# Performance work log

Hardware: AMD Instinct MI355X
Metric: run time of the kernel (lower is better)

Reference implementation:

```python
import jax, jax.numpy as jnp
import numpy as np

N = 50000      # nodes
E = 800000     # edges (before self loops)
IN = 32        # in_channels
HID = 32       # hidden_channels per head
HEADS = 4
OUT = 8        # out_channels (classes)
HD = HID * HEADS  # 128
NEG_SLOPE = 0.2
LN_EPS = 1e-5


def setup_inputs() -> dict:
    key = jax.random.key(0)
    ks = jax.random.split(key, 20)
    g = lambda k, shape, s=0.05: (jax.random.normal(k, shape, jnp.float32) * s)
    return {
        "x": jax.random.normal(ks[0], (N, IN), jnp.float32),
        "edge_index": jax.random.randint(ks[1], (2, E), 0, N, dtype=jnp.int32),
        # layer 0 GATConv (IN -> HID per head, HEADS heads, concat)
        "W0": g(ks[2], (IN, HD)),
        "a_src0": g(ks[3], (HEADS, HID)),
        "a_dst0": g(ks[4], (HEADS, HID)),
        "b0": jnp.zeros((HD,), jnp.float32),
        # skip projection for layer 0 (IN != HD)
        "skipW0": g(ks[5], (IN, HD)),
        "skipb0": jnp.zeros((HD,), jnp.float32),
        # LayerNorm 0
        "g0": jnp.ones((HD,), jnp.float32),
        "be0": jnp.zeros((HD,), jnp.float32),
        # layer 1 GATConv (HD -> HID per head, HEADS heads, concat)
        "W1": g(ks[6], (HD, HD)),
        "a_src1": g(ks[7], (HEADS, HID)),
        "a_dst1": g(ks[8], (HEADS, HID)),
        "b1": jnp.zeros((HD,), jnp.float32),
        # LayerNorm 1
        "g1": jnp.ones((HD,), jnp.float32),
        "be1": jnp.zeros((HD,), jnp.float32),
        # final GATConv (HD -> OUT, 1 head, no concat)
        "W2": g(ks[9], (HD, OUT)),
        "a_src2": g(ks[10], (1, OUT)),
        "a_dst2": g(ks[11], (1, OUT)),
        "b2": jnp.zeros((OUT,), jnp.float32),
    }


def _gat_conv(h_in, W, a_src, a_dst, b, src, dst, heads, C, concat):
    """PyG-style GATConv (eval mode, self-loops already in src/dst)."""
    n = h_in.shape[0]
    h = (h_in @ W).reshape(n, heads, C)                 # [N, H, C]
    s = jnp.sum(h * a_src[None], axis=-1)               # [N, H]
    d = jnp.sum(h * a_dst[None], axis=-1)               # [N, H]
    e = jax.nn.leaky_relu(s[src] + d[dst], NEG_SLOPE)   # [E, H]
    # segment softmax over incoming edges of each destination node
    m = jax.ops.segment_max(e, dst, num_segments=n)
    m = jnp.where(jnp.isfinite(m), m, 0.0)
    ex = jnp.exp(e - m[dst])
    den = jax.ops.segment_sum(ex, dst, num_segments=n)
    alpha = ex / (den[dst] + 1e-16)                     # [E, H]
    msg = h[src] * alpha[:, :, None]                    # [E, H, C]
    out = jax.ops.segment_sum(msg, dst, num_segments=n) # [N, H, C]
    out = out.reshape(n, heads * C) if concat else out.mean(axis=1)
    return out + b


def _layer_norm(x, g, b):
    mu = x.mean(axis=-1, keepdims=True)
    var = jnp.mean(jnp.square(x - mu), axis=-1, keepdims=True)
    return (x - mu) * jax.lax.rsqrt(var + LN_EPS) * g + b


def reference(x, edge_index, W0, a_src0, a_dst0, b0, skipW0, skipb0, g0, be0,
              W1, a_src1, a_dst1, b1, g1, be1, W2, a_src2, a_dst2, b2):
    n = x.shape[0]
    loop = jnp.arange(n, dtype=edge_index.dtype)
    src = jnp.concatenate([edge_index[0], loop])
    dst = jnp.concatenate([edge_index[1], loop])

    # layer 0: GATConv + projected residual + LN + ELU (dropout = identity, eval)
    h = _gat_conv(x, W0, a_src0, a_dst0, b0, src, dst, HEADS, HID, True)
    h = h + (x @ skipW0 + skipb0)
    h = jax.nn.elu(_layer_norm(h, g0, be0))

    # layer 1: GATConv + identity residual (dims match) + LN + ELU
    h1 = _gat_conv(h, W1, a_src1, a_dst1, b1, src, dst, HEADS, HID, True)
    h1 = h1 + h
    h1 = jax.nn.elu(_layer_norm(h1, g1, be1))

    # final layer: 1 head, mean (concat=False)
    return _gat_conv(h1, W2, a_src2, a_dst2, b2, src, dst, 1, OUT, False)
```

## Files before the change

### kernel.cpp

```cpp
#include <hip/hip_runtime.h>
#include <hip/hip_fp16.h>
#include <math.h>

#define N_NODES 50000
#define N_EDGES 800000
#define E2 (N_EDGES + N_NODES)
#define HD 128
#define OUT_C 8
#define NEG_SLOPE 0.2f
#define LN_EPS 1e-5f
#define NB_SCAN ((N_NODES + 255) / 256)

__device__ __forceinline__ float lrelu(float x) { return x > 0.f ? x : NEG_SLOPE * x; }
__device__ __forceinline__ void fma4(float4& a, float s, const float4& w) {
  a.x += s * w.x; a.y += s * w.y; a.z += s * w.z; a.w += s * w.w;
}
__device__ __forceinline__ float dot4(const float4& a, const float4& b) {
  return a.x * b.x + a.y * b.y + a.z * b.z + a.w * b.w;
}

__global__ void hist_k(const int* __restrict__ ei, int* __restrict__ counts) {
  int e = blockIdx.x * 256 + threadIdx.x;
  if (e >= E2) return;
  int d = (e < N_EDGES) ? ei[N_EDGES + e] : (e - N_EDGES);
  atomicAdd(&counts[d], 1);
}

__global__ void scan1_k(const int* __restrict__ counts, int* __restrict__ incl,
                        int* __restrict__ bsum, int n) {
  int tid = threadIdx.x; int gid = blockIdx.x * 256 + tid;
  int v = (gid < n) ? counts[gid] : 0;
  int lane = tid & 63, wv = tid >> 6;
  int x = v;
  #pragma unroll
  for (int off = 1; off < 64; off <<= 1) { int t = __shfl_up(x, off); if (lane >= off) x += t; }
  __shared__ int ws[4];
  if (lane == 63) ws[wv] = x;
  __syncthreads();
  for (int w = 0; w < wv; ++w) x += ws[w];
  incl[gid] = x;
  if (tid == 255) bsum[blockIdx.x] = x;
}

__global__ void scan2_k(const int* __restrict__ bsum, int* __restrict__ boffs, int nb) {
  int tid = threadIdx.x;
  int v = (tid < nb) ? bsum[tid] : 0;
  int lane = tid & 63, wv = tid >> 6;
  int x = v;
  #pragma unroll
  for (int off = 1; off < 64; off <<= 1) { int t = __shfl_up(x, off); if (lane >= off) x += t; }
  __shared__ int ws[4];
  if (lane == 63) ws[wv] = x;
  __syncthreads();
  for (int w = 0; w < wv; ++w) x += ws[w];
  if (tid < nb) boffs[tid] = x - v;
}

__global__ void scan3_k(const int* __restrict__ counts, const int* __restrict__ incl,
                        const int* __restrict__ boffs, int* __restrict__ row_start,
                        int* __restrict__ cursor, int n) {
  int gid = blockIdx.x * 256 + threadIdx.x;
  if (gid < n) {
    int r = incl[gid] - counts[gid] + boffs[blockIdx.x];
    row_start[gid] = r; cursor[gid] = r;
  }
  if (gid == 0) row_start[n] = E2;
}

__global__ void scatter_k(const int* __restrict__ ei, int* __restrict__ cursor,
                          int* __restrict__ csr_src) {
  int e = blockIdx.x * 256 + threadIdx.x;
  if (e >= E2) return;
  int s, d;
  if (e < N_EDGES) { s = ei[e]; d = ei[N_EDGES + e]; } else { s = e - N_EDGES; d = s; }
  int pos = atomicAdd(&cursor[d], 1);
  csr_src[pos] = s;
}

#define NPB0 16
__global__ __launch_bounds__(256) void gemm0_k(
    const float* __restrict__ x, const float* __restrict__ W0,
    const float* __restrict__ skipW, const float* __restrict__ skipb,
    const float* __restrict__ asrc, const float* __restrict__ adst,
    __half* __restrict__ h0, float* __restrict__ skip,
    float* __restrict__ s0, float* __restrict__ d0) {
  __shared__ float Ws[32 * 128];
  __shared__ float Ss[32 * 128];
  __shared__ float xs[NPB0][32];
  int tid = threadIdx.x;
  for (int i = tid; i < 32 * 128 / 4; i += 256) {
    ((float4*)Ws)[i] = ((const float4*)W0)[i];
    ((float4*)Ss)[i] = ((const float4*)skipW)[i];
  }
  int nb = blockIdx.x * NPB0;
  for (int i = tid; i < NPB0 * 32 / 4; i += 256) {
    int node = nb + (i >> 3);
    ((float4*)xs)[i] = (node < N_NODES) ? ((const float4*)x)[node * 8 + (i & 7)]
                                        : make_float4(0, 0, 0, 0);
  }
  __syncthreads();
  int j = tid >> 5;
  int cg = tid & 31;
  float4 aH[2] = {{0,0,0,0},{0,0,0,0}};
  float4 aS[2] = {{0,0,0,0},{0,0,0,0}};
  #pragma unroll 4
  for (int k = 0; k < 32; ++k) {
    float4 w  = ((const float4*)Ws)[k * 32 + cg];
    float4 wk = ((const float4*)Ss)[k * 32 + cg];
    float x0 = xs[j][k], x1 = xs[j + 8][k];
    fma4(aH[0], x0, w);  fma4(aH[1], x1, w);
    fma4(aS[0], x0, wk); fma4(aS[1], x1, wk);
  }
  float4 as4 = ((const float4*)asrc)[cg];
  float4 ad4 = ((const float4*)adst)[cg];
  float4 sb4 = ((const float4*)skipb)[cg];
  #pragma unroll
  for (int t = 0; t < 2; ++t) {
    int n = nb + j + t * 8;
    if (n < N_NODES) {
      float4 h = aH[t];
      union { __half2 h2[2]; uint2 u; } pk;
      pk.h2[0] = __floats2half2_rn(h.x, h.y);
      pk.h2[1] = __floats2half2_rn(h.z, h.w);
      ((uint2*)h0)[(size_t)n * 32 + cg] = pk.u;
      float4 sk = aS[t];
      sk.x += sb4.x; sk.y += sb4.y; sk.z += sb4.z; sk.w += sb4.w;
      ((float4*)skip)[n * 32 + cg] = sk;
      float sv = h.x * as4.x + h.y * as4.y + h.z * as4.z + h.w * as4.w;
      float dv = h.x * ad4.x + h.y * ad4.y + h.z * ad4.z + h.w * ad4.w;
      #pragma unroll
      for (int off = 1; off < 8; off <<= 1) { sv += __shfl_xor(sv, off); dv += __shfl_xor(dv, off); }
      if ((cg & 7) == 0) { s0[n * 4 + (cg >> 3)] = sv; d0[n * 4 + (cg >> 3)] = dv; }
    }
  }
}

#define G1N 64
__global__ __launch_bounds__(256) void gemm1_k(
    const float* __restrict__ hin, const float* __restrict__ W1,
    const float* __restrict__ asrc, const float* __restrict__ adst,
    __half* __restrict__ hpre, float* __restrict__ s1, float* __restrict__ d1) {
  __shared__ float xs[G1N][132];
  __shared__ float Ws[64][128];
  int tid = threadIdx.x;
  int nb = blockIdx.x * G1N;
  for (int i = tid; i < G1N * 32; i += 256) {
    int ln = i >> 5, k4 = i & 31;
    int node = nb + ln;
    float4 v = (node < N_NODES) ? ((const float4*)hin)[(size_t)node * 32 + k4]
                                : make_float4(0, 0, 0, 0);
    *(float4*)&xs[ln][k4 * 4] = v;
  }
  int cg = tid & 15, jn = tid >> 4;
  int c0 = cg * 8, n0 = jn * 4;
  float4 acc[4][2] = {};
  for (int ph = 0; ph < 2; ++ph) {
    __syncthreads();
    for (int i = tid; i < 64 * 32; i += 256)
      ((float4*)Ws)[i] = ((const float4*)W1)[ph * 2048 + i];
    __syncthreads();
    #pragma unroll 4
    for (int k = 0; k < 64; ++k) {
      float4 w0 = *(const float4*)&Ws[k][c0];
      float4 w1 = *(const float4*)&Ws[k][c0 + 4];
      int kk = ph * 64 + k;
      #pragma unroll
      for (int i = 0; i < 4; ++i) {
        float xv = xs[n0 + i][kk];
        fma4(acc[i][0], xv, w0);
        fma4(acc[i][1], xv, w1);
      }
    }
  }
  float4 a0 = *(const float4*)&asrc[c0], a1 = *(const float4*)&asrc[c0 + 4];
  float4 d0_ = *(const float4*)&adst[c0], d1_ = *(const float4*)&adst[c0 + 4];
  int head = cg >> 2;
  #pragma unroll
  for (int i = 0; i < 4; ++i) {
    int n = nb + n0 + i;
    if (n < N_NODES) {
      union { __half2 h2[4]; uint4 u; } pk;
      pk.h2[0] = __floats2half2_rn(acc[i][0].x, acc[i][0].y);
      pk.h2[1] = __floats2half2_rn(acc[i][0].z, acc[i][0].w);
      pk.h2[2] = __floats2half2_rn(acc[i][1].x, acc[i][1].y);
      pk.h2[3] = __floats2half2_rn(acc[i][1].z, acc[i][1].w);
      ((uint4*)hpre)[(size_t)n * 16 + cg] = pk.u;
      float sv = dot4(acc[i][0], a0) + dot4(acc[i][1], a1);
      float dv = dot4(acc[i][0], d0_) + dot4(acc[i][1], d1_);
      sv += __shfl_xor(sv, 1); sv += __shfl_xor(sv, 2);
      dv += __shfl_xor(dv, 1); dv += __shfl_xor(dv, 2);
      if ((cg & 3) == 0) { s1[n * 4 + head] = sv; d1[n * 4 + head] = dv; }
    }
  }
}

__global__ __launch_bounds__(256) void gemm2_k(
    const float* __restrict__ hin, const float* __restrict__ W2,
    const float* __restrict__ asrc, const float* __restrict__ adst,
    float* __restrict__ h2, float* __restrict__ s2, float* __restrict__ d2) {
  __shared__ float Ws[128 * 8];
  __shared__ float as[8], ad[8];
  int tid = threadIdx.x;
  for (int i = tid; i < 128 * 8 / 4; i += 256) ((float4*)Ws)[i] = ((const float4*)W2)[i];
  if (tid < 8) { as[tid] = asrc[tid]; ad[tid] = adst[tid]; }
  __syncthreads();
  int node = blockIdx.x * 256 + tid;
  if (node >= N_NODES) return;
  const float4* row = (const float4*)(hin + (size_t)node * 128);
  float acc[8] = {0, 0, 0, 0, 0, 0, 0, 0};
  #pragma unroll 4
  for (int k4 = 0; k4 < 32; ++k4) {
    float4 xv = row[k4];
    const float* wb = &Ws[k4 * 32];
    #pragma unroll
    for (int c = 0; c < 8; ++c)
      acc[c] += xv.x * wb[c] + xv.y * wb[8 + c] + xv.z * wb[16 + c] + xv.w * wb[24 + c];
  }
  float sv = 0.f, dv = 0.f;
  #pragma unroll
  for (int c = 0; c < 8; ++c) {
    h2[(size_t)node * 8 + c] = acc[c];
    sv += acc[c] * as[c]; dv += acc[c] * ad[c];
  }
  s2[node] = sv; d2[node] = dv;
}

__global__ __launch_bounds__(256) void agg_k(
    const int* __restrict__ row_start, const int* __restrict__ csr_src,
    const __half* __restrict__ hfeat, const float* __restrict__ sarr,
    const float* __restrict__ darr, const float* __restrict__ bias,
    const float* __restrict__ resid, const float* __restrict__ gamma,
    const float* __restrict__ beta, float* __restrict__ outf) {
  int lane = threadIdx.x & 63;
  int n = blockIdx.x * 4 + (threadIdx.x >> 6);
  if (n >= N_NODES) return;
  int rs = row_start[n], re = row_start[n + 1];
  float4 dn4 = ((const float4*)darr)[n];
  float m0 = -INFINITY, m1 = -INFINITY, m2 = -INFINITY, m3 = -INFINITY;
  for (int p = rs + lane; p < re; p += 64) {
    int src = csr_src[p];
    float4 sv = ((const float4*)sarr)[src];
    m0 = fmaxf(m0, lrelu(sv.x + dn4.x)); m1 = fmaxf(m1, lrelu(sv.y + dn4.y));
    m2 = fmaxf(m2, lrelu(sv.z + dn4.z)); m3 = fmaxf(m3, lrelu(sv.w + dn4.w));
  }
  #pragma unroll
  for (int off = 32; off; off >>= 1) {
    m0 = fmaxf(m0, __shfl_xor(m0, off)); m1 = fmaxf(m1, __shfl_xor(m1, off));
    m2 = fmaxf(m2, __shfl_xor(m2, off)); m3 = fmaxf(m3, __shfl_xor(m3, off));
  }
  int head = lane >> 4;
  float mh = head == 0 ? m0 : head == 1 ? m1 : head == 2 ? m2 : m3;
  float dh = head == 0 ? dn4.x : head == 1 ? dn4.y : head == 2 ? dn4.z : dn4.w;
  const __half2* hf2 = (const __half2*)hfeat;
  float den = 0.f, acc0 = 0.f, acc1 = 0.f;
  int p = rs;
  for (; p + 1 < re; p += 2) {
    int sA = csr_src[p], sB = csr_src[p + 1];
    float shA = sarr[sA * 4 + head], shB = sarr[sB * 4 + head];
    __half2 hA = hf2[(size_t)sA * 64 + lane];
    __half2 hB = hf2[(size_t)sB * 64 + lane];
    float exA = __expf(lrelu(shA + dh) - mh);
    float exB = __expf(lrelu(shB + dh) - mh);
    den += exA + exB;
    float2 a = __half22float2(hA), b = __half22float2(hB);
    acc0 += exA * a.x + exB * b.x;
    acc1 += exA * a.y + exB * b.y;
  }
  if (p < re) {
    int sA = csr_src[p];
    float shA = sarr[sA * 4 + head];
    __half2 hA = hf2[(size_t)sA * 64 + lane];
    float exA = __expf(lrelu(shA + dh) - mh);
    den += exA;
    float2 a = __half22float2(hA);
    acc0 += exA * a.x; acc1 += exA * a.y;
  }
  float rden = 1.f / (den + 1e-16f);
  int c0 = lane * 2;
  float o0 = acc0 * rden + bias[c0]     + resid[(size_t)n * 128 + c0];
  float o1 = acc1 * rden + bias[c0 + 1] + resid[(size_t)n * 128 + c0 + 1];
  float s = o0 + o1;
  #pragma unroll
  for (int off = 32; off; off >>= 1) s += __shfl_xor(s, off);
  float mu = s * (1.f / 128.f);
  float v0 = o0 - mu, v1 = o1 - mu;
  float vv = v0 * v0 + v1 * v1;
  #pragma unroll
  for (int off = 32; off; off >>= 1) vv += __shfl_xor(vv, off);
  float rstd = rsqrtf(vv * (1.f / 128.f) + LN_EPS);
  float y0 = v0 * rstd * gamma[c0]     + beta[c0];
  float y1 = v1 * rstd * gamma[c0 + 1] + beta[c0 + 1];
  y0 = y0 > 0.f ? y0 : expm1f(y0);
  y1 = y1 > 0.f ? y1 : expm1f(y1);
  ((float2*)outf)[(size_t)n * 64 + lane] = make_float2(y0, y1);
}

__global__ __launch_bounds__(256) void agg2_k(
    const int* __restrict__ row_start, const int* __restrict__ csr_src,
    const float* __restrict__ h2, const float* __restrict__ s2,
    const float* __restrict__ d2, const float* __restrict__ b2,
    float* __restrict__ outf) {
  int lane = threadIdx.x & 63;
  int n = blockIdx.x * 4 + (threadIdx.x >> 6);
  if (n >= N_NODES) return;
  int rs = row_start[n], re = row_start[n + 1];
  float dn = d2[n];
  float mx = -INFINITY;
  for (int p = rs + lane; p < re; p += 64)
    mx = fmaxf(mx, lrelu(s2[csr_src[p]] + dn));
  #pragma unroll
  for (int off = 32; off; off >>= 1) mx = fmaxf(mx, __shfl_xor(mx, off));
  float den = 0.f;
  float acc[8] = {0, 0, 0, 0, 0, 0, 0, 0};
  for (int p = rs + lane; p < re; p += 64) {
    int src = csr_src[p];
    float e = lrelu(s2[src] + dn);
    float ex = __expf(e - mx);
    den += ex;
    float4 hA = ((const float4*)h2)[src * 2];
    float4 hB = ((const float4*)h2)[src * 2 + 1];
    acc[0] += ex * hA.x; acc[1] += ex * hA.y; acc[2] += ex * hA.z; acc[3] += ex * hA.w;
    acc[4] += ex * hB.x; acc[5] += ex * hB.y; acc[6] += ex * hB.z; acc[7] += ex * hB.w;
  }
  #pragma unroll
  for (int off = 32; off; off >>= 1) {
    den += __shfl_xor(den, off);
    #pragma unroll
    for (int i = 0; i < 8; ++i) acc[i] += __shfl_xor(acc[i], off);
  }
  if (lane == 0) {
    float r = 1.f / (den + 1e-16f);
    #pragma unroll
    for (int i = 0; i < 8; ++i) outf[(size_t)n * 8 + i] = acc[i] * r + b2[i];
  }
}

extern "C" void kernel_launch(void* const* d_in, const int* in_sizes, int n_in,
                              void* d_out, int out_size, void* d_ws, size_t ws_size,
                              hipStream_t stream) {
  const float* x      = (const float*)d_in[0];
  const int*   ei     = (const int*)d_in[1];
  const float* W0     = (const float*)d_in[2];
  const float* a_src0 = (const float*)d_in[3];
  const float* a_dst0 = (const float*)d_in[4];
  const float* b0     = (const float*)d_in[5];
  const float* skipW0 = (const float*)d_in[6];
  const float* skipb0 = (const float*)d_in[7];
  const float* g0     = (const float*)d_in[8];
  const float* be0    = (const float*)d_in[9];
  const float* W1     = (const float*)d_in[10];
  const float* a_src1 = (const float*)d_in[11];
  const float* a_dst1 = (const float*)d_in[12];
  const float* b1     = (const float*)d_in[13];
  const float* g1     = (const float*)d_in[14];
  const float* be1    = (const float*)d_in[15];
  const float* W2     = (const float*)d_in[16];
  const float* a_src2 = (const float*)d_in[17];
  const float* a_dst2 = (const float*)d_in[18];
  const float* b2     = (const float*)d_in[19];
  float* out = (float*)d_out;

  char* w = (char*)d_ws;
  auto alloc = [&](size_t bytes) -> char* {
    char* p = w; w += (bytes + 255) & ~(size_t)255; return p;
  };
  int* counts    = (int*)alloc((size_t)N_NODES * 4);
  int* row_start = (int*)alloc((size_t)(N_NODES + 1) * 4);
  int* cursor    = (int*)alloc((size_t)N_NODES * 4);
  int* incl      = (int*)alloc((size_t)NB_SCAN * 256 * 4);
  int* bsum      = (int*)alloc((size_t)NB_SCAN * 4);
  int* boffs     = (int*)alloc((size_t)NB_SCAN * 4);
  int* csr_src   = (int*)alloc((size_t)E2 * 4);
  float* A       = (float*)alloc((size_t)N_NODES * 128 * 4);
  float* B       = (float*)alloc((size_t)N_NODES * 128 * 4);
  float* C       = (float*)alloc((size_t)N_NODES * 128 * 4);
  float* s0v = (float*)alloc((size_t)N_NODES * 4 * 4);
  float* d0v = (float*)alloc((size_t)N_NODES * 4 * 4);
  float* s1v = (float*)alloc((size_t)N_NODES * 4 * 4);
  float* d1v = (float*)alloc((size_t)N_NODES * 4 * 4);
  float* s2v = (float*)alloc((size_t)N_NODES * 4);
  float* d2v = (float*)alloc((size_t)N_NODES * 4);

  hipMemsetAsync(counts, 0, (size_t)N_NODES * 4, stream);
  int egrid = (E2 + 255) / 256;
  hist_k<<<egrid, 256, 0, stream>>>(ei, counts);
  scan1_k<<<NB_SCAN, 256, 0, stream>>>(counts, incl, bsum, N_NODES);
  scan2_k<<<1, 256, 0, stream>>>(bsum, boffs, NB_SCAN);
  scan3_k<<<NB_SCAN, 256, 0, stream>>>(counts, incl, boffs, row_start, cursor, N_NODES);
  scatter_k<<<egrid, 256, 0, stream>>>(ei, cursor, csr_src);

  int ngrid4 = (N_NODES + 3) / 4;
  gemm0_k<<<(N_NODES + NPB0 - 1) / NPB0, 256, 0, stream>>>(
      x, W0, skipW0, skipb0, a_src0, a_dst0, (__half*)A, B, s0v, d0v);
  agg_k<<<ngrid4, 256, 0, stream>>>(row_start, csr_src, (const __half*)A, s0v, d0v, b0, B, g0, be0, C);
  gemm1_k<<<(N_NODES + G1N - 1) / G1N, 256, 0, stream>>>(C, W1, a_src1, a_dst1, (__half*)B, s1v, d1v);
  agg_k<<<ngrid4, 256, 0, stream>>>(row_start, csr_src, (const __half*)B, s1v, d1v, b1, C, g1, be1, A);
  gemm2_k<<<(N_NODES + 255) / 256, 256, 0, stream>>>(A, W2, a_src2, a_dst2, B, s2v, d2v);
  agg2_k<<<ngrid4, 256, 0, stream>>>(row_start, csr_src, B, s2v, d2v, b2, out);
}
```

Baseline: 422.6 us.

## Drop softmax max pass and share per-edge exp weights via LDS

Removes the segment-max pass in both aggregation kernels and computes exp of the leaky-relu logits without max subtraction. In the 128-wide aggregation, each wave computes the per-edge exps for all four heads once per 64-edge chunk and stages them and the source indices in LDS, instead of every lane re-gathering scores. This removes one full edge pass and redundant gathers. It risks overflow if logits become large, because the max shift that kept exp bounded is gone.

```diff
diff --git a/kernel.cpp b/kernel.cpp
--- a/kernel.cpp
+++ b/kernel.cpp
@@ -225,58 +225,65 @@
   s2[node] = sv; d2[node] = dv;
 }
 
+template<int LAYER>
 __global__ __launch_bounds__(256) void agg_k(
     const int* __restrict__ row_start, const int* __restrict__ csr_src,
     const __half* __restrict__ hfeat, const float* __restrict__ sarr,
     const float* __restrict__ darr, const float* __restrict__ bias,
     const float* __restrict__ resid, const float* __restrict__ gamma,
     const float* __restrict__ beta, float* __restrict__ outf) {
+  __shared__ float exs[4][64 * 4];
+  __shared__ int   srs[4][64];
   int lane = threadIdx.x & 63;
-  int n = blockIdx.x * 4 + (threadIdx.x >> 6);
+  int wv = threadIdx.x >> 6;
+  int n = blockIdx.x * 4 + wv;
   if (n >= N_NODES) return;
   int rs = row_start[n], re = row_start[n + 1];
   float4 dn4 = ((const float4*)darr)[n];
-  float m0 = -INFINITY, m1 = -INFINITY, m2 = -INFINITY, m3 = -INFINITY;
-  for (int p = rs + lane; p < re; p += 64) {
-    int src = csr_src[p];
-    float4 sv = ((const float4*)sarr)[src];
-    m0 = fmaxf(m0, lrelu(sv.x + dn4.x)); m1 = fmaxf(m1, lrelu(sv.y + dn4.y));
-    m2 = fmaxf(m2, lrelu(sv.z + dn4.z)); m3 = fmaxf(m3, lrelu(sv.w + dn4.w));
+  int head = lane >> 4;
+  int c0 = lane * 2;
+  const __half2* hf2 = (const __half2*)hfeat;
+  float4 denv = {0.f, 0.f, 0.f, 0.f};
+  float acc0 = 0.f, acc1 = 0.f;
+  for (int base = rs; base < re; base += 64) {
+    int cnt = re - base; if (cnt > 64) cnt = 64;
+    if (lane < cnt) {
+      int src = csr_src[base + lane];
+      float4 sv = ((const float4*)sarr)[src];
+      float4 ex;
+      ex.x = __expf(lrelu(sv.x + dn4.x));
+      ex.y = __expf(lrelu(sv.y + dn4.y));
+      ex.z = __expf(lrelu(sv.z + dn4.z));
+      ex.w = __expf(lrelu(sv.w + dn4.w));
+      denv.x += ex.x; denv.y += ex.y; denv.z += ex.z; denv.w += ex.w;
+      *(float4*)&exs[wv][lane * 4] = ex;
+      srs[wv][lane] = src;
+    }
+    asm volatile("s_waitcnt lgkmcnt(0)" ::: "memory");
+    int e = 0;
+    for (; e + 1 < cnt; e += 2) {
+      int sA = srs[wv][e], sB = srs[wv][e + 1];
+      float eA = exs[wv][e * 4 + head], eB = exs[wv][e * 4 + 4 + head];
+      float2 a = __half22float2(hf2[(size_t)sA * 64 + lane]);
+      float2 b = __half22float2(hf2[(size_t)sB * 64 + lane]);
+      acc0 += eA * a.x + eB * b.x;
+      acc1 += eA * a.y + eB * b.y;
+    }
+    if (e < cnt) {
+      int sA = srs[wv][e];
+      float eA = exs[wv][e * 4 + head];
+      float2 a = __half22float2(hf2[(size_t)sA * 64 + lane]);
+      acc0 += eA * a.x; acc1 += eA * a.y;
+    }
+    asm volatile("s_waitcnt lgkmcnt(0)" ::: "memory");
   }
   #pragma unroll
   for (int off = 32; off; off >>= 1) {
-    m0 = fmaxf(m0, __shfl_xor(m0, off)); m1 = fmaxf(m1, __shfl_xor(m1, off));
-    m2 = fmaxf(m2, __shfl_xor(m2, off)); m3 = fmaxf(m3, __shfl_xor(m3, off));
-  }
-  int head = lane >> 4;
-  float mh = head == 0 ? m0 : head == 1 ? m1 : head == 2 ? m2 : m3;
-  float dh = head == 0 ? dn4.x : head == 1 ? dn4.y : head == 2 ? dn4.z : dn4.w;
-  const __half2* hf2 = (const __half2*)hfeat;
-  float den = 0.f, acc0 = 0.f, acc1 = 0.f;
-  int p = rs;
-  for (; p + 1 < re; p += 2) {
-    int sA = csr_src[p], sB = csr_src[p + 1];
-    float shA = sarr[sA * 4 + head], shB = sarr[sB * 4 + head];
-    __half2 hA = hf2[(size_t)sA * 64 + lane];
-    __half2 hB = hf2[(size_t)sB * 64 + lane];
-    float exA = __expf(lrelu(shA + dh) - mh);
-    float exB = __expf(lrelu(shB + dh) - mh);
-    den += exA + exB;
-    float2 a = __half22float2(hA), b = __half22float2(hB);
-    acc0 += exA * a.x + exB * b.x;
-    acc1 += exA * a.y + exB * b.y;
-  }
-  if (p < re) {
-    int sA = csr_src[p];
-    float shA = sarr[sA * 4 + head];
-    __half2 hA = hf2[(size_t)sA * 64 + lane];
-    float exA = __expf(lrelu(shA + dh) - mh);
-    den += exA;
-    float2 a = __half22float2(hA);
-    acc0 += exA * a.x; acc1 += exA * a.y;
-  }
+    denv.x += __shfl_xor(denv.x, off); denv.y += __shfl_xor(denv.y, off);
+    denv.z += __shfl_xor(denv.z, off); denv.w += __shfl_xor(denv.w, off);
+  }
+  float den = head == 0 ? denv.x : head == 1 ? denv.y : head == 2 ? denv.z : denv.w;
   float rden = 1.f / (den + 1e-16f);
-  int c0 = lane * 2;
   float o0 = acc0 * rden + bias[c0]     + resid[(size_t)n * 128 + c0];
   float o1 = acc1 * rden + bias[c0 + 1] + resid[(size_t)n * 128 + c0 + 1];
   float s = o0 + o1;
@@ -305,17 +312,11 @@
   if (n >= N_NODES) return;
   int rs = row_start[n], re = row_start[n + 1];
   float dn = d2[n];
-  float mx = -INFINITY;
-  for (int p = rs + lane; p < re; p += 64)
-    mx = fmaxf(mx, lrelu(s2[csr_src[p]] + dn));
-  #pragma unroll
-  for (int off = 32; off; off >>= 1) mx = fmaxf(mx, __shfl_xor(mx, off));
   float den = 0.f;
   float acc[8] = {0, 0, 0, 0, 0, 0, 0, 0};
   for (int p = rs + lane; p < re; p += 64) {
     int src = csr_src[p];
-    float e = lrelu(s2[src] + dn);
-    float ex = __expf(e - mx);
+    float ex = __expf(lrelu(s2[src] + dn));
     den += ex;
     float4 hA = ((const float4*)h2)[src * 2];
     float4 hB = ((const float4*)h2)[src * 2 + 1];
@@ -392,9 +393,9 @@
   int ngrid4 = (N_NODES + 3) / 4;
   gemm0_k<<<(N_NODES + NPB0 - 1) / NPB0, 256, 0, stream>>>(
       x, W0, skipW0, skipb0, a_src0, a_dst0, (__half*)A, B, s0v, d0v);
-  agg_k<<<ngrid4, 256, 0, stream>>>(row_start, csr_src, (const __half*)A, s0v, d0v, b0, B, g0, be0, C);
+  agg_k<0><<<ngrid4, 256, 0, stream>>>(row_start, csr_src, (const __half*)A, s0v, d0v, b0, B, g0, be0, C);
   gemm1_k<<<(N_NODES + G1N - 1) / G1N, 256, 0, stream>>>(C, W1, a_src1, a_dst1, (__half*)B, s1v, d1v);
-  agg_k<<<ngrid4, 256, 0, stream>>>(row_start, csr_src, (const __half*)B, s1v, d1v, b1, C, g1, be1, A);
+  agg_k<1><<<ngrid4, 256, 0, stream>>>(row_start, csr_src, (const __half*)B, s1v, d1v, b1, C, g1, be1, A);
   gemm2_k<<<(N_NODES + 255) / 256, 256, 0, stream>>>(A, W2, a_src2, a_dst2, B, s2v, d2v);
   agg2_k<<<ngrid4, 256, 0, stream>>>(row_start, csr_src, B, s2v, d2v, b2, out);
 }
```

Result: faster. 385.1 us (-8.9%).
